# Kernel optimization log

Measured on AMD Instinct MI355X. Metric: run time of the kernel, lower is better.

Reference implementation:

```python
import jax, jax.numpy as jnp
import numpy as np

L_POS, L_DIR, H = 10, 4, 128
N = 1048576

def posenc(x, L):
    feats = [x]
    for j in range(L):
        s = (2.0 ** j) * x
        feats.append(jnp.sin(s))
        feats.append(jnp.cos(s))
    return jnp.concatenate(feats, axis=1)

def _w(key, fan_in, fan_out):
    return jax.random.normal(key, (fan_in, fan_out), dtype=jnp.float32) * (1.0 / np.sqrt(fan_in))

def setup_inputs() -> dict:
    key = jax.random.key(0)
    ks = jax.random.split(key, 16)
    pos = jax.random.normal(ks[0], (N, 3), dtype=jnp.float32)
    dirs = jax.random.normal(ks[1], (N, 3), dtype=jnp.float32)
    d_pos = 3 + 2 * 3 * L_POS  # 63
    d_dir = 3 + 2 * 3 * L_DIR  # 27
    inp = {
        'pos': pos, 'dirs': dirs,
        # block1: 4 hidden layers, ReLU everywhere incl. output (bias-free tcnn MLP)
        'b1_w0': _w(ks[2], d_pos, H), 'b1_w1': _w(ks[3], H, H),
        'b1_w2': _w(ks[4], H, H),    'b1_w3': _w(ks[5], H, H),
        'b1_w4': _w(ks[6], H, H),
        # block2: 3 hidden layers, linear output of width H+1
        'b2_w0': _w(ks[7], H + d_pos, H), 'b2_w1': _w(ks[8], H, H),
        'b2_w2': _w(ks[9], H, H),         'b2_w3': _w(ks[10], H, H + 1),
        # block3: 1 hidden layer of H//2, sigmoid output of width 3
        'b3_w0': _w(ks[11], H + d_dir, H // 2), 'b3_w1': _w(ks[12], H // 2, 3),
    }
    return inp

def reference(pos, dirs, b1_w0, b1_w1, b1_w2, b1_w3, b1_w4,
              b2_w0, b2_w1, b2_w2, b2_w3, b3_w0, b3_w1):
    relu = jax.nn.relu
    x_emb = posenc(pos, L_POS)   # [N, 63]
    d_emb = posenc(dirs, L_DIR)  # [N, 27]
    # block1: ReLU hidden + ReLU output
    h = relu(x_emb @ b1_w0)
    h = relu(h @ b1_w1)
    h = relu(h @ b1_w2)
    h = relu(h @ b1_w3)
    h = relu(h @ b1_w4)          # [N, 128]
    # block2: ReLU hidden, linear output
    g = relu(jnp.concatenate([h, x_emb], axis=1) @ b2_w0)
    g = relu(g @ b2_w1)
    g = relu(g @ b2_w2)
    g = g @ b2_w3                # [N, 129]
    sigma = jax.nn.relu(g[:, -1])
    feat = g[:, :-1]             # [N, 128]
    # block3: ReLU hidden, sigmoid output
    c = relu(jnp.concatenate([feat, d_emb], axis=1) @ b3_w0)
    color = jax.nn.sigmoid(c @ b3_w1)  # [N, 3]
    return (color, sigma)
```

## Files before the change

kernel.cpp:

```cpp
#include <hip/hip_runtime.h>
#include <hip/hip_bf16.h>

#define NTOT  1048576
#define MWG   128
#define BLK   256
#define ROWB  384
#define ACT_BYTES  (MWG * ROWB)

typedef __attribute__((ext_vector_type(8))) short  bf16x8;
typedef __attribute__((ext_vector_type(4))) float  f32x4;

__device__ __forceinline__ void barL() {
  asm volatile("s_waitcnt lgkmcnt(0)\n\ts_barrier" ::: "memory");
}

__device__ __forceinline__ unsigned short f2bf(float f) {
  unsigned u = __float_as_uint(f);
  u += 0x7fffu + ((u >> 16) & 1u);
  return (unsigned short)(u >> 16);
}

__device__ __forceinline__ unsigned pk2bf(float lo, float hi) {
  float2 t; t.x = lo; t.y = hi;
  __hip_bfloat162 b = __float22bfloat162_rn(t);
  return *(unsigned*)&b;
}

__global__ __launch_bounds__(256) void prepack_k(
    const float* __restrict__ s0, const float* __restrict__ s1,
    const float* __restrict__ s2, const float* __restrict__ s3,
    const float* __restrict__ s4, const float* __restrict__ s5,
    const float* __restrict__ s6, const float* __restrict__ s7,
    const float* __restrict__ s8, const float* __restrict__ s9,
    const float* __restrict__ s10, unsigned short* __restrict__ dst)
{
  const int nw_[11]  = {128,128,128,128,128,128,128,128,144, 64, 16};
  const int kw_[11]  = { 64,128,128,128,128,192,128,128,128,192, 64};
  const int nc_[11]  = {128,128,128,128,128,128,128,128,129, 64,  3};
  const int k1_[11]  = { 63,128,128,128,128, 63,128,128,128, 27, 64};
  const int o1_[11]  = {  0,  0,  0,  0,  0,128,  0,  0,  0,128,  0};
  const int k2_[11]  = {999,999,999,999,999, 64,999,999,999, 64,999};
  const int do_[11]  = {0,8192,24576,40960,57344,73728,98304,114688,131072,149504,161792};

  int c = blockIdx.x;
  const float* src =
    c==0?s0: c==1?s1: c==2?s2: c==3?s3: c==4?s4: c==5?s5:
    c==6?s6: c==7?s7: c==8?s8: c==9?s9: s10;
  int nw=nw_[c], kw=kw_[c], nc=nc_[c], k1=k1_[c], o1=o1_[c], k2=k2_[c];
  int KS = kw >> 5;
  int total = nw * kw;
  for (int idx = blockIdx.y * blockDim.x + threadIdx.x; idx < total;
       idx += gridDim.y * blockDim.x) {
    int e   = idx & 7;
    int l15 = (idx >> 3) & 15;
    int lg  = (idx >> 7) & 3;
    int r   = idx >> 9;
    int ks  = r % KS;
    int nt  = r / KS;
    int n = nt * 16 + l15;
    int k = ks * 32 + lg * 8 + e;
    float v = 0.f;
    if (n < nc) {
      if (k < k1)       v = src[(o1 + k) * nc + n];
      else if (k >= k2) v = src[(k - k2) * nc + n];
    }
    dst[do_[c] + idx] = f2bf(v);
  }
}

template<int I0, int L>
__device__ __forceinline__ void posenc_store(unsigned char* actb, int row,
                                             float p0, float p1, float p2)
{
#pragma unroll
  for (int q = 0; q < 4; q++) {
    float hv[8];
#pragma unroll
    for (int e = 0; e < 8; e++) {
      const int i = I0 + q * 8 + e;
      float v;
      if (i == 0) v = p0;
      else if (i == 1) v = p1;
      else if (i == 2) v = p2;
      else {
        const int idx = i - 3, j = idx / 6, t = idx % 6;
        if (j < L) {
          const float sc = (float)(1 << j);
          const float a  = (t % 3 == 0 ? p0 : (t % 3 == 1 ? p1 : p2)) * sc;
          v = (t < 3) ? __sinf(a) : __cosf(a);
        } else v = 0.f;
      }
      hv[e] = v;
    }
    uint4 pk;
    pk.x = pk2bf(hv[0], hv[1]);
    pk.y = pk2bf(hv[2], hv[3]);
    pk.z = pk2bf(hv[4], hv[5]);
    pk.w = pk2bf(hv[6], hv[7]);
    int b = (row * ROWB + (I0 + q * 8) * 2) ^ ((row & 7) << 4);
    *(uint4*)(actb + b) = pk;
  }
}

template<int KSN>
__device__ __forceinline__ void preloadW1(bf16x8* pf, const unsigned short* wchunk,
                                          int lane, int wn)
{
  if (KSN == 0) return;
  const unsigned short* wl = wchunk + (wn * 4) * (KSN * 512) + lane * 8;
#pragma unroll
  for (int nt = 0; nt < 4; nt++)
    pf[nt] = *(const bf16x8*)(wl + (nt * KSN) * 512);
}

template<int KS, int KSN, int KB, int DST, bool RELU, bool MIDBAR, bool SIG>
__device__ __forceinline__ void layer22(
    unsigned char* actb, const unsigned short* __restrict__ wchunk,
    const unsigned short* __restrict__ wnext, bf16x8* pf,
    const unsigned (*rb2)[2], const unsigned (*wb2)[4],
    int lane, int wid, float* __restrict__ out, long grow0)
{
  const int l15 = lane & 15;
  const int lg  = lane >> 4;
  const int wn  = wid & 1;
  const unsigned short* wl = wchunk + (wn * 4) * (KS * 512) + lane * 8;
  const f32x4 vzero = {0.f, 0.f, 0.f, 0.f};
  f32x4 acc[4][4];

  {
    bf16x8 bfr4[4];
#pragma unroll
    for (int mq = 0; mq < 4; mq++)
      bfr4[mq] = *(const bf16x8*)(actb + rb2[mq][0] + KB * 2);
#pragma unroll
    for (int nt = 0; nt < 4; nt++)
#pragma unroll
      for (int mq = 0; mq < 4; mq++)
        acc[mq][nt] = __builtin_amdgcn_mfma_f32_16x16x32_bf16(
            pf[nt], bfr4[mq], vzero, 0, 0, 0);
  }
#pragma unroll
  for (int ks = 1; ks < KS; ks++) {
    bf16x8 afr[4];
#pragma unroll
    for (int nt = 0; nt < 4; nt++)
      afr[nt] = *(const bf16x8*)(wl + (nt * KS + ks) * 512);
    bf16x8 bfr4[4];
#pragma unroll
    for (int mq = 0; mq < 4; mq++)
      bfr4[mq] = *(const bf16x8*)(actb + rb2[mq][ks & 1] + (KB * 2 + (ks >> 1) * 128));
#pragma unroll
    for (int nt = 0; nt < 4; nt++)
#pragma unroll
      for (int mq = 0; mq < 4; mq++)
        acc[mq][nt] = __builtin_amdgcn_mfma_f32_16x16x32_bf16(
            afr[nt], bfr4[mq], acc[mq][nt], 0, 0, 0);
  }

  preloadW1<KSN>(pf, wnext, lane, wn);

  f32x4 accs[2];
  if (SIG) {
    accs[0] = vzero; accs[1] = vzero;
#pragma unroll
    for (int ks = 0; ks < KS; ks++) {
      bf16x8 afs = *(const bf16x8*)(wchunk + (8 * KS + ks) * 512 + lane * 8);
#pragma unroll
      for (int j = 0; j < 2; j++) {
        int m = (2 * wid + j) * 16 + l15;
        int byt = (m * ROWB + KB * 2 + ks * 64 + lg * 16) ^ ((m & 7) << 4);
        bf16x8 bfs = *(const bf16x8*)(actb + byt);
        accs[j] = __builtin_amdgcn_mfma_f32_16x16x32_bf16(afs, bfs, accs[j], 0, 0, 0);
      }
    }
  }

  if (MIDBAR) barL();

#pragma unroll
  for (int mq = 0; mq < 4; mq++) {
#pragma unroll
    for (int nt = 0; nt < 4; nt++) {
      f32x4 v = acc[mq][nt];
      if (RELU) {
        v.x = fmaxf(v.x, 0.f); v.y = fmaxf(v.y, 0.f);
        v.z = fmaxf(v.z, 0.f); v.w = fmaxf(v.w, 0.f);
      }
      uint2 pk;
      pk.x = pk2bf(v.x, v.y);
      pk.y = pk2bf(v.z, v.w);
      *(uint2*)(actb + wb2[mq][nt] + DST * 2) = pk;
    }
  }
  if (SIG && lg == 0) {
#pragma unroll
    for (int j = 0; j < 2; j++) {
      int m = (2 * wid + j) * 16 + l15;
      out[3L * NTOT + grow0 + m] = fmaxf(accs[j].x, 0.f);
    }
  }
  barL();
}

__device__ __forceinline__ void layer_b3w0(
    unsigned char* actb, const unsigned short* __restrict__ wchunk,
    int lane, int wid)
{
  const int l15 = lane & 15;
  const int lg  = lane >> 4;
  const unsigned short* wl = wchunk + wid * (6 * 512) + lane * 8;
  const f32x4 vzero = {0.f, 0.f, 0.f, 0.f};
  f32x4 acc[8];

  {
    bf16x8 afr = *(const bf16x8*)(wl);
#pragma unroll
    for (int mt = 0; mt < 8; mt++) {
      int m = mt * 16 + l15;
      int byt = (m * ROWB + lg * 16) ^ ((m & 7) << 4);
      bf16x8 b = *(const bf16x8*)(actb + byt);
      acc[mt] = __builtin_amdgcn_mfma_f32_16x16x32_bf16(afr, b, vzero, 0, 0, 0);
    }
  }
#pragma unroll
  for (int ks = 1; ks < 6; ks++) {
    bf16x8 afr = *(const bf16x8*)(wl + ks * 512);
#pragma unroll
    for (int mt = 0; mt < 8; mt++) {
      int m = mt * 16 + l15;
      int byt = (m * ROWB + ks * 64 + lg * 16) ^ ((m & 7) << 4);
      bf16x8 b = *(const bf16x8*)(actb + byt);
      acc[mt] = __builtin_amdgcn_mfma_f32_16x16x32_bf16(afr, b, acc[mt], 0, 0, 0);
    }
  }

  barL();

#pragma unroll
  for (int mt = 0; mt < 8; mt++) {
    f32x4 v = acc[mt];
    v.x = fmaxf(v.x, 0.f); v.y = fmaxf(v.y, 0.f);
    v.z = fmaxf(v.z, 0.f); v.w = fmaxf(v.w, 0.f);
    uint2 pk;
    pk.x = pk2bf(v.x, v.y);
    pk.y = pk2bf(v.z, v.w);
    int m = mt * 16 + l15;
    int byt = (m * ROWB + wid * 32 + lg * 8) ^ ((m & 7) << 4);
    *(uint2*)(actb + byt) = pk;
  }
  barL();
}

__device__ __forceinline__ void color_n(
    unsigned char* actb, const unsigned short* __restrict__ wchunk,
    int lane, int wid, float* __restrict__ out, long grow0)
{
  const int l15 = lane & 15;
  const int lg  = lane >> 4;
  const f32x4 vzero = {0.f, 0.f, 0.f, 0.f};
  f32x4 acc[2];
  int m0 = (2 * wid + 0) * 16 + l15;
  int m1 = (2 * wid + 1) * 16 + l15;
#pragma unroll
  for (int ks = 0; ks < 2; ks++) {
    bf16x8 afr = *(const bf16x8*)(wchunk + ks * 512 + lane * 8);
    int b0a = (m0 * ROWB + ks * 64 + lg * 16) ^ ((m0 & 7) << 4);
    int b1a = (m1 * ROWB + ks * 64 + lg * 16) ^ ((m1 & 7) << 4);
    bf16x8 b0 = *(const bf16x8*)(actb + b0a);
    bf16x8 b1 = *(const bf16x8*)(actb + b1a);
    if (ks == 0) {
      acc[0] = __builtin_amdgcn_mfma_f32_16x16x32_bf16(afr, b0, vzero, 0, 0, 0);
      acc[1] = __builtin_amdgcn_mfma_f32_16x16x32_bf16(afr, b1, vzero, 0, 0, 0);
    } else {
      acc[0] = __builtin_amdgcn_mfma_f32_16x16x32_bf16(afr, b0, acc[0], 0, 0, 0);
      acc[1] = __builtin_amdgcn_mfma_f32_16x16x32_bf16(afr, b1, acc[1], 0, 0, 0);
    }
  }
  if (lg == 0) {
#pragma unroll
    for (int j = 0; j < 2; j++) {
      int m = (2 * wid + j) * 16 + l15;
      long g3 = (grow0 + m) * 3;
      out[g3 + 0] = 1.f / (1.f + __expf(-acc[j].x));
      out[g3 + 1] = 1.f / (1.f + __expf(-acc[j].y));
      out[g3 + 2] = 1.f / (1.f + __expf(-acc[j].z));
    }
  }
}

__global__ __launch_bounds__(BLK, 2) void nerf_fused(
    const float* __restrict__ pos, const float* __restrict__ dirs,
    const unsigned short* __restrict__ wp, float* __restrict__ out)
{
  __shared__ unsigned char actb[ACT_BYTES];

  const int tid   = threadIdx.x;
  const int lane  = tid & 63;
  const int wid   = tid >> 6;
  const int wm    = wid >> 1;
  const int wn    = wid & 1;
  const long grow0 = (long)blockIdx.x * MWG;

  const int l15 = lane & 15;
  const int lg  = lane >> 4;

  unsigned rb2[4][2], wb2[4][4];
#pragma unroll
  for (int mq = 0; mq < 4; mq++) {
    int m = wm * 64 + mq * 16 + l15;
    unsigned sw = (unsigned)((m & 7) << 4);
    unsigned base = (unsigned)(m * ROWB);
    rb2[mq][0] = (base + lg * 16) ^ sw;
    rb2[mq][1] = (base + 64 + lg * 16) ^ sw;
#pragma unroll
    for (int nt = 0; nt < 4; nt++)
      wb2[mq][nt] = (base + wn * 128 + nt * 32 + lg * 8) ^ sw;
  }

  const int row = wid * 32 + (lane & 31);
  const long g  = grow0 + row;

  bf16x8 pf[4];
  preloadW1<2>(pf, wp + 0, lane, wn);

  {
    float p0 = pos[g * 3 + 0], p1 = pos[g * 3 + 1], p2 = pos[g * 3 + 2];
    if (lane < 32) posenc_store<0, 10>(actb, row, p0, p1, p2);
    else           posenc_store<32, 10>(actb, row, p0, p1, p2);
  }
  barL();

  layer22<2, 4, 0, 64, true, false, false>(actb, wp +      0, wp +   8192, pf, rb2, wb2, lane, wid, out, grow0);
  layer22<4, 4, 64, 64, true, true, false>(actb, wp +   8192, wp +  24576, pf, rb2, wb2, lane, wid, out, grow0);
  layer22<4, 4, 64, 64, true, true, false>(actb, wp +  24576, wp +  40960, pf, rb2, wb2, lane, wid, out, grow0);
  layer22<4, 4, 64, 64, true, true, false>(actb, wp +  40960, wp +  57344, pf, rb2, wb2, lane, wid, out, grow0);
  layer22<4, 6, 64, 64, true, true, false>(actb, wp +  57344, wp +  73728, pf, rb2, wb2, lane, wid, out, grow0);
  layer22<6, 4, 0, 64, true, true, false>(actb, wp +  73728, wp +  98304, pf, rb2, wb2, lane, wid, out, grow0);

  {
    float p0 = dirs[g * 3 + 0], p1 = dirs[g * 3 + 1], p2 = dirs[g * 3 + 2];
    if (lane < 32) posenc_store<0, 4>(actb, row, p0, p1, p2);
    else           posenc_store<32, 4>(actb, row, p0, p1, p2);
  }

  layer22<4, 4, 64, 64, true, true, false>(actb, wp +  98304, wp + 114688, pf, rb2, wb2, lane, wid, out, grow0);
  layer22<4, 4, 64, 64, true, true, false>(actb, wp + 114688, wp + 131072, pf, rb2, wb2, lane, wid, out, grow0);
  layer22<4, 0, 64, 64, false, true, true>(actb, wp + 131072, nullptr,     pf, rb2, wb2, lane, wid, out, grow0);
  layer_b3w0(actb, wp + 149504, lane, wid);
  color_n(actb, wp + 161792, lane, wid, out, grow0);
}

extern "C" void kernel_launch(void* const* d_in, const int* in_sizes, int n_in,
                              void* d_out, int out_size, void* d_ws, size_t ws_size,
                              hipStream_t stream)
{
  const float* pos  = (const float*)d_in[0];
  const float* dirs = (const float*)d_in[1];
  unsigned short* wpack = (unsigned short*)d_ws;
  float* out = (float*)d_out;

  prepack_k<<<dim3(11, 12, 1), 256, 0, stream>>>(
      (const float*)d_in[2], (const float*)d_in[3], (const float*)d_in[4],
      (const float*)d_in[5], (const float*)d_in[6], (const float*)d_in[7],
      (const float*)d_in[8], (const float*)d_in[9], (const float*)d_in[10],
      (const float*)d_in[11], (const float*)d_in[12], wpack);

  nerf_fused<<<NTOT / MWG, BLK, 0, stream>>>(pos, dirs, wpack, out);
}
```

Before: 326.0 us.

## Split each 128-row tile across 8 waves instead of 4

Doubles the block to 512 threads and gives each wave a 64x32 output slice instead of 64x64, so the accumulator and weight-fragment register footprint halves. The launch bound now requests 4 blocks per CU to raise wave occupancy and hide LDS and MFMA latency. Positional encoding stays on the first four waves. The b3 and color layers are re-split across eight waves. In exchange, each weight fragment is shared by fewer MFMAs, activation reads from LDS per MFMA go up, and barriers now synchronise more waves.

```diff
diff --git a/kernel.cpp b/kernel.cpp
--- a/kernel.cpp
+++ b/kernel.cpp
@@ -3,7 +3,7 @@
 
 #define NTOT  1048576
 #define MWG   128
-#define BLK   256
+#define BLK   512
 #define ROWB  384
 #define ACT_BYTES  (MWG * ROWB)
 
@@ -107,9 +107,9 @@
                                           int lane, int wn)
 {
   if (KSN == 0) return;
-  const unsigned short* wl = wchunk + (wn * 4) * (KSN * 512) + lane * 8;
-#pragma unroll
-  for (int nt = 0; nt < 4; nt++)
+  const unsigned short* wl = wchunk + (wn * 2) * (KSN * 512) + lane * 8;
+#pragma unroll
+  for (int nt = 0; nt < 2; nt++)
     pf[nt] = *(const bf16x8*)(wl + (nt * KSN) * 512);
 }
 
@@ -117,15 +117,15 @@
 __device__ __forceinline__ void layer22(
     unsigned char* actb, const unsigned short* __restrict__ wchunk,
     const unsigned short* __restrict__ wnext, bf16x8* pf,
-    const unsigned (*rb2)[2], const unsigned (*wb2)[4],
+    const unsigned (*rb2)[2], const unsigned (*wb2)[2],
     int lane, int wid, float* __restrict__ out, long grow0)
 {
   const int l15 = lane & 15;
   const int lg  = lane >> 4;
-  const int wn  = wid & 1;
-  const unsigned short* wl = wchunk + (wn * 4) * (KS * 512) + lane * 8;
+  const int wn  = wid & 3;
+  const unsigned short* wl = wchunk + (wn * 2) * (KS * 512) + lane * 8;
   const f32x4 vzero = {0.f, 0.f, 0.f, 0.f};
-  f32x4 acc[4][4];
+  f32x4 acc[4][2];
 
   {
     bf16x8 bfr4[4];
@@ -133,7 +133,7 @@
     for (int mq = 0; mq < 4; mq++)
       bfr4[mq] = *(const bf16x8*)(actb + rb2[mq][0] + KB * 2);
 #pragma unroll
-    for (int nt = 0; nt < 4; nt++)
+    for (int nt = 0; nt < 2; nt++)
 #pragma unroll
       for (int mq = 0; mq < 4; mq++)
         acc[mq][nt] = __builtin_amdgcn_mfma_f32_16x16x32_bf16(
@@ -141,16 +141,16 @@
   }
 #pragma unroll
   for (int ks = 1; ks < KS; ks++) {
-    bf16x8 afr[4];
-#pragma unroll
-    for (int nt = 0; nt < 4; nt++)
+    bf16x8 afr[2];
+#pragma unroll
+    for (int nt = 0; nt < 2; nt++)
       afr[nt] = *(const bf16x8*)(wl + (nt * KS + ks) * 512);
     bf16x8 bfr4[4];
 #pragma unroll
     for (int mq = 0; mq < 4; mq++)
       bfr4[mq] = *(const bf16x8*)(actb + rb2[mq][ks & 1] + (KB * 2 + (ks >> 1) * 128));
 #pragma unroll
-    for (int nt = 0; nt < 4; nt++)
+    for (int nt = 0; nt < 2; nt++)
 #pragma unroll
       for (int mq = 0; mq < 4; mq++)
         acc[mq][nt] = __builtin_amdgcn_mfma_f32_16x16x32_bf16(
@@ -159,19 +159,16 @@
 
   preloadW1<KSN>(pf, wnext, lane, wn);
 
-  f32x4 accs[2];
+  f32x4 accs;
   if (SIG) {
-    accs[0] = vzero; accs[1] = vzero;
+    accs = vzero;
 #pragma unroll
     for (int ks = 0; ks < KS; ks++) {
       bf16x8 afs = *(const bf16x8*)(wchunk + (8 * KS + ks) * 512 + lane * 8);
-#pragma unroll
-      for (int j = 0; j < 2; j++) {
-        int m = (2 * wid + j) * 16 + l15;
-        int byt = (m * ROWB + KB * 2 + ks * 64 + lg * 16) ^ ((m & 7) << 4);
-        bf16x8 bfs = *(const bf16x8*)(actb + byt);
-        accs[j] = __builtin_amdgcn_mfma_f32_16x16x32_bf16(afs, bfs, accs[j], 0, 0, 0);
-      }
+      int m = wid * 16 + l15;
+      int byt = (m * ROWB + KB * 2 + ks * 64 + lg * 16) ^ ((m & 7) << 4);
+      bf16x8 bfs = *(const bf16x8*)(actb + byt);
+      accs = __builtin_amdgcn_mfma_f32_16x16x32_bf16(afs, bfs, accs, 0, 0, 0);
     }
   }
 
@@ -180,7 +177,7 @@
 #pragma unroll
   for (int mq = 0; mq < 4; mq++) {
 #pragma unroll
-    for (int nt = 0; nt < 4; nt++) {
+    for (int nt = 0; nt < 2; nt++) {
       f32x4 v = acc[mq][nt];
       if (RELU) {
         v.x = fmaxf(v.x, 0.f); v.y = fmaxf(v.y, 0.f);
@@ -193,11 +190,8 @@
     }
   }
   if (SIG && lg == 0) {
-#pragma unroll
-    for (int j = 0; j < 2; j++) {
-      int m = (2 * wid + j) * 16 + l15;
-      out[3L * NTOT + grow0 + m] = fmaxf(accs[j].x, 0.f);
-    }
+    int m = wid * 16 + l15;
+    out[3L * NTOT + grow0 + m] = fmaxf(accs.x, 0.f);
   }
   barL();
 }
@@ -208,15 +202,17 @@
 {
   const int l15 = lane & 15;
   const int lg  = lane >> 4;
-  const unsigned short* wl = wchunk + wid * (6 * 512) + lane * 8;
+  const int nt4 = wid & 3;
+  const int mh  = wid >> 2;
+  const unsigned short* wl = wchunk + nt4 * (6 * 512) + lane * 8;
   const f32x4 vzero = {0.f, 0.f, 0.f, 0.f};
-  f32x4 acc[8];
+  f32x4 acc[4];
 
   {
     bf16x8 afr = *(const bf16x8*)(wl);
 #pragma unroll
-    for (int mt = 0; mt < 8; mt++) {
-      int m = mt * 16 + l15;
+    for (int mt = 0; mt < 4; mt++) {
+      int m = mh * 64 + mt * 16 + l15;
       int byt = (m * ROWB + lg * 16) ^ ((m & 7) << 4);
       bf16x8 b = *(const bf16x8*)(actb + byt);
       acc[mt] = __builtin_amdgcn_mfma_f32_16x16x32_bf16(afr, b, vzero, 0, 0, 0);
@@ -226,8 +222,8 @@
   for (int ks = 1; ks < 6; ks++) {
     bf16x8 afr = *(const bf16x8*)(wl + ks * 512);
 #pragma unroll
-    for (int mt = 0; mt < 8; mt++) {
-      int m = mt * 16 + l15;
+    for (int mt = 0; mt < 4; mt++) {
+      int m = mh * 64 + mt * 16 + l15;
       int byt = (m * ROWB + ks * 64 + lg * 16) ^ ((m & 7) << 4);
       bf16x8 b = *(const bf16x8*)(actb + byt);
       acc[mt] = __builtin_amdgcn_mfma_f32_16x16x32_bf16(afr, b, acc[mt], 0, 0, 0);
@@ -237,15 +233,15 @@
   barL();
 
 #pragma unroll
-  for (int mt = 0; mt < 8; mt++) {
+  for (int mt = 0; mt < 4; mt++) {
     f32x4 v = acc[mt];
     v.x = fmaxf(v.x, 0.f); v.y = fmaxf(v.y, 0.f);
     v.z = fmaxf(v.z, 0.f); v.w = fmaxf(v.w, 0.f);
     uint2 pk;
     pk.x = pk2bf(v.x, v.y);
     pk.y = pk2bf(v.z, v.w);
-    int m = mt * 16 + l15;
-    int byt = (m * ROWB + wid * 32 + lg * 8) ^ ((m & 7) << 4);
+    int m = mh * 64 + mt * 16 + l15;
+    int byt = (m * ROWB + nt4 * 32 + lg * 8) ^ ((m & 7) << 4);
     *(uint2*)(actb + byt) = pk;
   }
   barL();
@@ -258,37 +254,25 @@
   const int l15 = lane & 15;
   const int lg  = lane >> 4;
   const f32x4 vzero = {0.f, 0.f, 0.f, 0.f};
-  f32x4 acc[2];
-  int m0 = (2 * wid + 0) * 16 + l15;
-  int m1 = (2 * wid + 1) * 16 + l15;
+  f32x4 acc;
+  int m = wid * 16 + l15;
 #pragma unroll
   for (int ks = 0; ks < 2; ks++) {
     bf16x8 afr = *(const bf16x8*)(wchunk + ks * 512 + lane * 8);
-    int b0a = (m0 * ROWB + ks * 64 + lg * 16) ^ ((m0 & 7) << 4);
-    int b1a = (m1 * ROWB + ks * 64 + lg * 16) ^ ((m1 & 7) << 4);
-    bf16x8 b0 = *(const bf16x8*)(actb + b0a);
-    bf16x8 b1 = *(const bf16x8*)(actb + b1a);
-    if (ks == 0) {
-      acc[0] = __builtin_amdgcn_mfma_f32_16x16x32_bf16(afr, b0, vzero, 0, 0, 0);
-      acc[1] = __builtin_amdgcn_mfma_f32_16x16x32_bf16(afr, b1, vzero, 0, 0, 0);
-    } else {
-      acc[0] = __builtin_amdgcn_mfma_f32_16x16x32_bf16(afr, b0, acc[0], 0, 0, 0);
-      acc[1] = __builtin_amdgcn_mfma_f32_16x16x32_bf16(afr, b1, acc[1], 0, 0, 0);
-    }
+    int ba = (m * ROWB + ks * 64 + lg * 16) ^ ((m & 7) << 4);
+    bf16x8 b = *(const bf16x8*)(actb + ba);
+    if (ks == 0) acc = __builtin_amdgcn_mfma_f32_16x16x32_bf16(afr, b, vzero, 0, 0, 0);
+    else         acc = __builtin_amdgcn_mfma_f32_16x16x32_bf16(afr, b, acc, 0, 0, 0);
   }
   if (lg == 0) {
-#pragma unroll
-    for (int j = 0; j < 2; j++) {
-      int m = (2 * wid + j) * 16 + l15;
-      long g3 = (grow0 + m) * 3;
-      out[g3 + 0] = 1.f / (1.f + __expf(-acc[j].x));
-      out[g3 + 1] = 1.f / (1.f + __expf(-acc[j].y));
-      out[g3 + 2] = 1.f / (1.f + __expf(-acc[j].z));
-    }
-  }
-}
-
-__global__ __launch_bounds__(BLK, 2) void nerf_fused(
+    long g3 = (grow0 + m) * 3;
+    out[g3 + 0] = 1.f / (1.f + __expf(-acc.x));
+    out[g3 + 1] = 1.f / (1.f + __expf(-acc.y));
+    out[g3 + 2] = 1.f / (1.f + __expf(-acc.z));
+  }
+}
+
+__global__ __launch_bounds__(BLK, 4) void nerf_fused(
     const float* __restrict__ pos, const float* __restrict__ dirs,
     const unsigned short* __restrict__ wp, float* __restrict__ out)
 {
@@ -297,14 +281,14 @@
   const int tid   = threadIdx.x;
   const int lane  = tid & 63;
   const int wid   = tid >> 6;
-  const int wm    = wid >> 1;
-  const int wn    = wid & 1;
+  const int wm    = wid >> 2;
+  const int wn    = wid & 3;
   const long grow0 = (long)blockIdx.x * MWG;
 
   const int l15 = lane & 15;
   const int lg  = lane >> 4;
 
-  unsigned rb2[4][2], wb2[4][4];
+  unsigned rb2[4][2], wb2[4][2];
 #pragma unroll
   for (int mq = 0; mq < 4; mq++) {
     int m = wm * 64 + mq * 16 + l15;
@@ -313,17 +297,16 @@
     rb2[mq][0] = (base + lg * 16) ^ sw;
     rb2[mq][1] = (base + 64 + lg * 16) ^ sw;
 #pragma unroll
-    for (int nt = 0; nt < 4; nt++)
-      wb2[mq][nt] = (base + wn * 128 + nt * 32 + lg * 8) ^ sw;
-  }
-
-  const int row = wid * 32 + (lane & 31);
-  const long g  = grow0 + row;
-
-  bf16x8 pf[4];
+    for (int nt = 0; nt < 2; nt++)
+      wb2[mq][nt] = (base + (wn * 2 + nt) * 32 + lg * 8) ^ sw;
+  }
+
+  bf16x8 pf[2];
   preloadW1<2>(pf, wp + 0, lane, wn);
 
-  {
+  if (wid < 4) {
+    int row = wid * 32 + (lane & 31);
+    long g  = grow0 + row;
     float p0 = pos[g * 3 + 0], p1 = pos[g * 3 + 1], p2 = pos[g * 3 + 2];
     if (lane < 32) posenc_store<0, 10>(actb, row, p0, p1, p2);
     else           posenc_store<32, 10>(actb, row, p0, p1, p2);
@@ -337,7 +320,9 @@
   layer22<4, 6, 64, 64, true, true, false>(actb, wp +  57344, wp +  73728, pf, rb2, wb2, lane, wid, out, grow0);
   layer22<6, 4, 0, 64, true, true, false>(actb, wp +  73728, wp +  98304, pf, rb2, wb2, lane, wid, out, grow0);
 
-  {
+  if (wid < 4) {
+    int row = wid * 32 + (lane & 31);
+    long g  = grow0 + row;
     float p0 = dirs[g * 3 + 0], p1 = dirs[g * 3 + 1], p2 = dirs[g * 3 + 2];
     if (lane < 32) posenc_store<0, 4>(actb, row, p0, p1, p2);
     else           posenc_store<32, 4>(actb, row, p0, p1, p2);
```

Result: slower. 355.6 us (+9.1%).
